# Optimization experiments

Hardware: AMD Instinct MI355X
Metric: run time of the kernel (lower is better)

Reference implementation:

```python
import jax, jax.numpy as jnp
import numpy as np

B, T, C, H = 2, 2048, 1024, 16
D = C // H
SCALE = 1.0 / np.sqrt(D).astype(np.float32)


def setup_inputs() -> dict:
    key = jax.random.key(0)
    kx, kq, kk, kv, ko = jax.random.split(key, 5)
    s = 1.0 / np.sqrt(C).astype(np.float32)
    return {
        "x": jax.random.normal(kx, (B, T, C), dtype=jnp.float32),
        "wq": jax.random.normal(kq, (C, C), dtype=jnp.float32) * s,
        "wk": jax.random.normal(kk, (C, C), dtype=jnp.float32) * s,
        "wv": jax.random.normal(kv, (C, C), dtype=jnp.float32) * s,
        "wo": jax.random.normal(ko, (C, C), dtype=jnp.float32) * s,
    }


def reference(x, wq, wk, wv, wo):
    # nn.Linear(y) = y @ W.T; weights stored [out, in]
    q = (x @ wq.T).reshape(B, T, H, D).transpose(0, 2, 1, 3)  # [B,H,T,D]
    k = (x @ wk.T).reshape(B, T, H, D).transpose(0, 2, 1, 3)
    v = (x @ wv.T).reshape(B, T, H, D).transpose(0, 2, 1, 3)
    scores = jnp.einsum("bhqd,bhkd->bhqk", q, k) * SCALE  # [B,H,T,T]
    causal = jnp.tril(jnp.ones((T, T), dtype=bool))
    scores = jnp.where(causal, scores, -jnp.inf)
    attn = jax.nn.softmax(scores, axis=-1)
    out = jnp.einsum("bhqk,bhkd->bhqd", attn, v)  # [B,H,T,D]
    out = out.transpose(0, 2, 1, 3).reshape(B, T, C)
    return out @ wo.T
```

## Files before the change

### kernel.cpp

```cpp
#include <hip/hip_runtime.h>
#include <hip/hip_bf16.h>

#define B_ 2
#define T_ 2048
#define C_ 1024
#define H_ 16
#define D_ 64
#define M_ (B_*T_)
#define SCALE_ 0.125f
#define LOG2E_ 1.44269504f
#define NEG_ (-1e30f)
#define THR_ 8.0f

typedef __bf16 bf16;
typedef __bf16 bf16x4 __attribute__((ext_vector_type(4)));
typedef __bf16 bf16x8 __attribute__((ext_vector_type(8)));
typedef float  f32x4  __attribute__((ext_vector_type(4)));

#define XB_ELEMS  ((size_t)M_*C_)
#define W_ELEMS   ((size_t)C_*C_)

__device__ __forceinline__ void glds16(const void* g, void* l) {
  __builtin_amdgcn_global_load_lds((const __attribute__((address_space(1))) void*)g,
                                   (__attribute__((address_space(3))) void*)l,
                                   16, 0, 0);
}

__global__ __launch_bounds__(256)
void cvt5(const float* __restrict__ x,  const float* __restrict__ wq,
          const float* __restrict__ wk, const float* __restrict__ wv,
          const float* __restrict__ wo, bf16* __restrict__ out,
          bf16* __restrict__ wodst) {
  int bid = blockIdx.x;
  const float* src; bf16* dst; size_t off;
  if (bid < 2048)      { src = x;  dst = out;                         off = (size_t)bid*2048; }
  else if (bid < 2560) { src = wq; dst = out + XB_ELEMS;              off = (size_t)(bid-2048)*2048; }
  else if (bid < 3072) { src = wk; dst = out + XB_ELEMS +   W_ELEMS;  off = (size_t)(bid-2560)*2048; }
  else if (bid < 3584) { src = wv; dst = out + XB_ELEMS + 2*W_ELEMS;  off = (size_t)(bid-3072)*2048; }
  else                 { src = wo; dst = wodst;                       off = (size_t)(bid-3584)*2048; }
  size_t i = off + (size_t)threadIdx.x * 8;
  f32x4 lo = *(const f32x4*)(src + i);
  f32x4 hi = *(const f32x4*)(src + i + 4);
  bf16x8 r;
  #pragma unroll
  for (int t = 0; t < 4; ++t) { r[t] = (bf16)lo[t]; r[t+4] = (bf16)hi[t]; }
  *(bf16x8*)(dst + i) = r;
}

template<int OUTMODE>
__global__ __launch_bounds__(256)
void gemm_nt(const bf16* __restrict__ Ab,
             const bf16* __restrict__ W0, const bf16* __restrict__ W1,
             const bf16* __restrict__ W2,
             void* __restrict__ O0v, void* __restrict__ O1v, void* __restrict__ O2v,
             int K) {
  __shared__ __align__(16) bf16 As[128*64];
  __shared__ __align__(16) bf16 Bs[128*64];

  const bf16* W = W0;
  void* Ov = O0v;
  bool vtrans = false;
  float oscale = 1.0f;
  if constexpr (OUTMODE == 0) {
    if (blockIdx.z == 0)      { oscale = SCALE_ * LOG2E_; }
    else if (blockIdx.z == 1) { W = W1; Ov = O1v; }
    else                      { W = W2; Ov = O2v; vtrans = true; }
  }

  const int m0 = blockIdx.y * 128, n0 = blockIdx.x * 128;
  const int tid = threadIdx.x, wid = tid >> 6, lane = tid & 63;
  const int wm = wid >> 1, wn = wid & 1;
  const int l15 = lane & 15, grp = lane >> 4;

  f32x4 acc[4][4] = {};

  const int lr8 = lane >> 3;
  const int lkswz = ((lane & 7) ^ lr8) * 8;
  const bf16* Ag = Ab + (size_t)(m0 + wid*8 + lr8) * K + lkswz;
  const bf16* Bg = W  + (size_t)(n0 + wid*8 + lr8) * K + lkswz;

  const int amRow = wm*64 + l15;
  const int bnRow = wn*64 + l15;
  const int swz = l15 & 7;

  for (int k0 = 0; k0 < K; k0 += 64) {
    __syncthreads();
    #pragma unroll
    for (int c = 0; c < 4; ++c) {
      glds16(Ag + (size_t)(c*32)*K + k0, As + (wid + c*4)*512);
      glds16(Bg + (size_t)(c*32)*K + k0, Bs + (wid + c*4)*512);
    }
    __syncthreads();

    #pragma unroll
    for (int ks = 0; ks < 2; ++ks) {
      const int aslot = ((ks*4 + grp) ^ swz) * 8;
      bf16x8 af[4], bfr[4];
      #pragma unroll
      for (int i = 0; i < 4; ++i) {
        af[i]  = *(const bf16x8*)(As + (amRow + i*16)*64 + aslot);
        bfr[i] = *(const bf16x8*)(Bs + (bnRow + i*16)*64 + aslot);
      }
      __builtin_amdgcn_s_setprio(1);
      #pragma unroll
      for (int i = 0; i < 4; ++i)
        #pragma unroll
        for (int j = 0; j < 4; ++j)
          acc[i][j] = __builtin_amdgcn_mfma_f32_16x16x32_bf16(af[i], bfr[j], acc[i][j], 0, 0, 0);
      __builtin_amdgcn_s_setprio(0);
    }
  }

  const int rBase = m0 + wm*64 + grp * 4;
  const int cBase = n0 + wn*64 + l15;
  #pragma unroll
  for (int fm = 0; fm < 4; ++fm) {
    #pragma unroll
    for (int fn = 0; fn < 4; ++fn) {
      #pragma unroll
      for (int j = 0; j < 4; ++j) {
        int m = rBase + fm*16 + j;
        int n = cBase + fn*16;
        if constexpr (OUTMODE == 0) {
          int b = m >> 11, t = m & 2047, h = n >> 6, d = n & 63;
          size_t idx = vtrans ? (((size_t)(b*H_ + h) * D_ + d) * T_ + t)
                              : (((size_t)(b*H_ + h) * T_ + t) * D_ + d);
          ((bf16*)Ov)[idx] = (bf16)(acc[fm][fn][j] * oscale);
        } else {
          ((float*)Ov)[(size_t)m * C_ + n] = acc[fm][fn][j];
        }
      }
    }
  }
}

#define LKV 72

__global__ __launch_bounds__(256)
void attn_fwd(const bf16* __restrict__ Q, const bf16* __restrict__ Km,
              const bf16* __restrict__ Vt, bf16* __restrict__ Oa) {
  __shared__ __align__(16) bf16 Ks [64*LKV];
  __shared__ __align__(16) bf16 Vts[64*LKV];
  __shared__ __align__(16) bf16 Ps [64*LKV];

  const int id = blockIdx.x;
  const int qt = 31 - (id >> 5);
  const int bh = id & 31;
  const int q0 = qt * 64;
  const int tid = threadIdx.x, wid = tid >> 6, lane = tid & 63;
  const int l15 = lane & 15;
  const int grp = lane >> 4;
  const int myrow4 = grp * 4;

  const bf16* Qb = Q  + (size_t)bh * T_ * D_;
  const bf16* Kb = Km + (size_t)bh * T_ * D_;
  const bf16* Vb = Vt + (size_t)bh * D_ * T_;

  const int ksr = tid >> 3, kskc = tid & 7;
  const int kSlot = grp * 8;
  const int b = bh >> 4, h = bh & 15;

  const int qrow = q0 + wid*16 + l15;
  bf16x8 aq0 = *(const bf16x8*)(Qb + (size_t)qrow*64 +      grp*8);
  bf16x8 aq1 = *(const bf16x8*)(Qb + (size_t)qrow*64 + 32 + grp*8);

  f32x4 oacc[4] = {};
  float m_s = NEG_, l_s = 0.f;

  bf16x8 kv_a = *(const bf16x8*)(Kb + (size_t)(ksr)*64      + kskc*8);
  bf16x8 kv_b = *(const bf16x8*)(Kb + (size_t)(ksr + 32)*64 + kskc*8);
  bf16x8 vt_a = *(const bf16x8*)(Vb + (size_t)(ksr     )*T_ + kskc*8);
  bf16x8 vt_b = *(const bf16x8*)(Vb + (size_t)(ksr + 32)*T_ + kskc*8);

  for (int kt = 0; kt <= qt; ++kt) {
    const int kv0 = kt * 64;

    __syncthreads();
    *(bf16x8*)(Ks  + ksr*LKV      + kskc*8) = kv_a;
    *(bf16x8*)(Ks  + (ksr+32)*LKV + kskc*8) = kv_b;
    *(bf16x8*)(Vts + ksr*LKV      + kskc*8) = vt_a;
    *(bf16x8*)(Vts + (ksr+32)*LKV + kskc*8) = vt_b;
    __syncthreads();

    {
      const int kn = (kt < qt) ? kv0 + 64 : kv0;
      kv_a = *(const bf16x8*)(Kb + (size_t)(kn + ksr)*64      + kskc*8);
      kv_b = *(const bf16x8*)(Kb + (size_t)(kn + ksr + 32)*64 + kskc*8);
      vt_a = *(const bf16x8*)(Vb + (size_t)(ksr     )*T_ + kn + kskc*8);
      vt_b = *(const bf16x8*)(Vb + (size_t)(ksr + 32)*T_ + kn + kskc*8);
    }

    f32x4 s[4];
    __builtin_amdgcn_s_setprio(1);
    #pragma unroll
    for (int n = 0; n < 4; ++n) {
      int row = n*16 + l15;
      bf16x8 bk0 = *(const bf16x8*)(Ks + row*LKV      + kSlot);
      bf16x8 bk1 = *(const bf16x8*)(Ks + row*LKV + 32 + kSlot);
      f32x4 a = {};
      a = __builtin_amdgcn_mfma_f32_16x16x32_bf16(bk0, aq0, a, 0, 0, 0);
      a = __builtin_amdgcn_mfma_f32_16x16x32_bf16(bk1, aq1, a, 0, 0, 0);
      s[n] = a;
    }
    __builtin_amdgcn_s_setprio(0);

    float pmax = NEG_;
    if (kt == qt) {
      #pragma unroll
      for (int n = 0; n < 4; ++n)
        #pragma unroll
        for (int j = 0; j < 4; ++j) {
          int kvg = kv0 + n*16 + myrow4 + j;
          float sv = (kvg <= qrow) ? s[n][j] : NEG_;
          s[n][j] = sv;
          pmax = fmaxf(pmax, sv);
        }
    } else {
      #pragma unroll
      for (int n = 0; n < 4; ++n)
        #pragma unroll
        for (int j = 0; j < 4; ++j) pmax = fmaxf(pmax, s[n][j]);
    }
    pmax = fmaxf(pmax, __shfl_xor(pmax, 16));
    pmax = fmaxf(pmax, __shfl_xor(pmax, 32));

    if (__any(pmax > m_s + THR_)) {
      float mnew = fmaxf(m_s, pmax);
      float scold = __builtin_amdgcn_exp2f(m_s - mnew);
      m_s = mnew;
      l_s *= scold;
      #pragma unroll
      for (int j = 0; j < 4; ++j) {
        float scj = __shfl(scold, myrow4 + j);
        #pragma unroll
        for (int n = 0; n < 4; ++n) oacc[n][j] *= scj;
      }
    }

    float ps = 0.f;
    #pragma unroll
    for (int n = 0; n < 4; ++n) {
      bf16x4 pw;
      #pragma unroll
      for (int j = 0; j < 4; ++j) {
        float p = __builtin_amdgcn_exp2f(s[n][j] - m_s);
        ps += p;
        pw[j] = (bf16)p;
      }
      *(bf16x4*)(Ps + (size_t)(wid*16 + l15)*LKV + n*16 + myrow4) = pw;
    }
    ps += __shfl_xor(ps, 16);
    ps += __shfl_xor(ps, 32);
    l_s += ps;

    asm volatile("s_waitcnt lgkmcnt(0)" ::: "memory");
    __builtin_amdgcn_sched_barrier(0);

    int parow = wid*16 + l15;
    bf16x8 pa0 = *(const bf16x8*)(Ps + parow*LKV      + kSlot);
    bf16x8 pa1 = *(const bf16x8*)(Ps + parow*LKV + 32 + kSlot);
    __builtin_amdgcn_s_setprio(1);
    #pragma unroll
    for (int n = 0; n < 4; ++n) {
      int vrow = n*16 + l15;
      bf16x8 bv0 = *(const bf16x8*)(Vts + vrow*LKV      + kSlot);
      bf16x8 bv1 = *(const bf16x8*)(Vts + vrow*LKV + 32 + kSlot);
      oacc[n] = __builtin_amdgcn_mfma_f32_16x16x32_bf16(pa0, bv0, oacc[n], 0, 0, 0);
      oacc[n] = __builtin_amdgcn_mfma_f32_16x16x32_bf16(pa1, bv1, oacc[n], 0, 0, 0);
    }
    __builtin_amdgcn_s_setprio(0);
  }

  const int tg = q0 + wid*16 + myrow4;
  #pragma unroll
  for (int j = 0; j < 4; ++j) {
    float lj = __shfl(l_s, myrow4 + j);
    float inv = 1.f / lj;
    int trow = tg + j;
    #pragma unroll
    for (int n = 0; n < 4; ++n) {
      int ch = h*64 + n*16 + l15;
      Oa[((size_t)(b*T_ + trow)) * C_ + ch] = (bf16)(oacc[n][j] * inv);
    }
  }
}

extern "C" void kernel_launch(void* const* d_in, const int* in_sizes, int n_in,
                              void* d_out, int out_size, void* d_ws, size_t ws_size,
                              hipStream_t stream) {
  const float* x  = (const float*)d_in[0];
  const float* wq = (const float*)d_in[1];
  const float* wk = (const float*)d_in[2];
  const float* wv = (const float*)d_in[3];
  const float* wo = (const float*)d_in[4];

  bf16* q  = (bf16*)d_ws;
  bf16* k  = q  + XB_ELEMS;
  bf16* v  = k  + XB_ELEMS;

  bf16* cvtbuf = (bf16*)d_out;
  bf16* xb  = cvtbuf;
  bf16* wqb = cvtbuf + XB_ELEMS;
  bf16* wkb = wqb + W_ELEMS;
  bf16* wvb = wkb + W_ELEMS;
  bf16* wob_stage = wvb + W_ELEMS;

  const bool bigws = ws_size >= (4*XB_ELEMS + W_ELEMS) * sizeof(bf16);
  bf16* ao  = bigws ? (v + XB_ELEMS) : xb;
  bf16* wob = bigws ? (v + XB_ELEMS + XB_ELEMS) : wob_stage;

  dim3 blk(256);
  cvt5<<<dim3(4096), blk, 0, stream>>>(x, wq, wk, wv, wo, cvtbuf, wob);
  gemm_nt<0><<<dim3(C_/128, M_/128, 3), blk, 0, stream>>>(xb, wqb, wkb, wvb,
                                                          q, k, v, C_);
  attn_fwd<<<dim3(1024), blk, 0, stream>>>(q, k, v, ao);
  bf16* aoSrc = ao;
  if (!bigws) {
    hipMemcpyAsync(q, xb,        XB_ELEMS * sizeof(bf16), hipMemcpyDeviceToDevice, stream);
    hipMemcpyAsync(k, wob_stage, W_ELEMS  * sizeof(bf16), hipMemcpyDeviceToDevice, stream);
    aoSrc = q; wob = k;
  }
  gemm_nt<1><<<dim3(C_/128, M_/128, 1), blk, 0, stream>>>(aoSrc, wob, nullptr, nullptr,
                                                          d_out, nullptr, nullptr, C_);
}
```

Before: 113.2 us.

## Split causal attention over KV range into two halves with combine kernel

Splits each query tile's causal KV loop into two roughly equal halves run by separate blocks (2048 blocks instead of 1024). Each half writes an unnormalized bf16 partial output plus per-row max and sum, and a new combine kernel merges them with log-sum-exp weights into the attention output. This targets load imbalance and low occupancy from the triangular causal work. In exchange it adds an extra kernel launch, an extra round trip of partial outputs through memory, and a larger workspace requirement; otherwise it falls back to the old path.

```diff
diff --git a/kernel.cpp b/kernel.cpp
--- a/kernel.cpp
+++ b/kernel.cpp
@@ -19,6 +19,8 @@
 
 #define XB_ELEMS  ((size_t)M_*C_)
 #define W_ELEMS   ((size_t)C_*C_)
+#define NSLOT     2048
+#define ML_FLOATS ((size_t)NSLOT*64*2)
 
 __device__ __forceinline__ void glds16(const void* g, void* l) {
   __builtin_amdgcn_global_load_lds((const __attribute__((address_space(1))) void*)g,
@@ -137,6 +139,202 @@
 #define LKV 72
 
 __global__ __launch_bounds__(256)
+void attn_split(const bf16* __restrict__ Q, const bf16* __restrict__ Km,
+                const bf16* __restrict__ Vt, bf16* __restrict__ pO,
+                float* __restrict__ ml) {
+  __shared__ __align__(16) bf16 Ks [64*LKV];
+  __shared__ __align__(16) bf16 Vts[64*LKV];
+  __shared__ __align__(16) bf16 Ps [64*LKV];
+
+  const int id = blockIdx.x;
+  const int qt = 31 - (id >> 6);
+  const int half = (id >> 5) & 1;
+  const int bh = id & 31;
+  const int q0 = qt * 64;
+  const int nl = (qt >> 1) + 1;
+  const int k0t = half ? nl : 0;
+  const int k1t = half ? (qt + 1) : nl;
+  const int slot = (qt*32 + bh)*2 + half;
+
+  const int tid = threadIdx.x, wid = tid >> 6, lane = tid & 63;
+  const int l15 = lane & 15;
+  const int grp = lane >> 4;
+  const int myrow4 = grp * 4;
+
+  if (k0t >= k1t) {
+    if (grp == 0 && wid < 4) {
+      int row = wid*16 + l15;
+      ml[(size_t)slot*128 + row*2    ] = NEG_;
+      ml[(size_t)slot*128 + row*2 + 1] = 0.f;
+    }
+    return;
+  }
+
+  const bf16* Qb = Q  + (size_t)bh * T_ * D_;
+  const bf16* Kb = Km + (size_t)bh * T_ * D_;
+  const bf16* Vb = Vt + (size_t)bh * D_ * T_;
+
+  const int ksr = tid >> 3, kskc = tid & 7;
+  const int kSlot = grp * 8;
+
+  const int qrow = q0 + wid*16 + l15;
+  bf16x8 aq0 = *(const bf16x8*)(Qb + (size_t)qrow*64 +      grp*8);
+  bf16x8 aq1 = *(const bf16x8*)(Qb + (size_t)qrow*64 + 32 + grp*8);
+
+  f32x4 oacc[4] = {};
+  float m_s = NEG_, l_s = 0.f;
+
+  const int kvS = k0t * 64;
+  bf16x8 kv_a = *(const bf16x8*)(Kb + (size_t)(kvS + ksr)*64      + kskc*8);
+  bf16x8 kv_b = *(const bf16x8*)(Kb + (size_t)(kvS + ksr + 32)*64 + kskc*8);
+  bf16x8 vt_a = *(const bf16x8*)(Vb + (size_t)(ksr     )*T_ + kvS + kskc*8);
+  bf16x8 vt_b = *(const bf16x8*)(Vb + (size_t)(ksr + 32)*T_ + kvS + kskc*8);
+
+  for (int kt = k0t; kt < k1t; ++kt) {
+    const int kv0 = kt * 64;
+
+    __syncthreads();
+    *(bf16x8*)(Ks  + ksr*LKV      + kskc*8) = kv_a;
+    *(bf16x8*)(Ks  + (ksr+32)*LKV + kskc*8) = kv_b;
+    *(bf16x8*)(Vts + ksr*LKV      + kskc*8) = vt_a;
+    *(bf16x8*)(Vts + (ksr+32)*LKV + kskc*8) = vt_b;
+    __syncthreads();
+
+    {
+      const int kn = (kt + 1 < k1t) ? kv0 + 64 : kv0;
+      kv_a = *(const bf16x8*)(Kb + (size_t)(kn + ksr)*64      + kskc*8);
+      kv_b = *(const bf16x8*)(Kb + (size_t)(kn + ksr + 32)*64 + kskc*8);
+      vt_a = *(const bf16x8*)(Vb + (size_t)(ksr     )*T_ + kn + kskc*8);
+      vt_b = *(const bf16x8*)(Vb + (size_t)(ksr + 32)*T_ + kn + kskc*8);
+    }
+
+    f32x4 s[4];
+    __builtin_amdgcn_s_setprio(1);
+    #pragma unroll
+    for (int n = 0; n < 4; ++n) {
+      int row = n*16 + l15;
+      bf16x8 bk0 = *(const bf16x8*)(Ks + row*LKV      + kSlot);
+      bf16x8 bk1 = *(const bf16x8*)(Ks + row*LKV + 32 + kSlot);
+      f32x4 a = {};
+      a = __builtin_amdgcn_mfma_f32_16x16x32_bf16(bk0, aq0, a, 0, 0, 0);
+      a = __builtin_amdgcn_mfma_f32_16x16x32_bf16(bk1, aq1, a, 0, 0, 0);
+      s[n] = a;
+    }
+    __builtin_amdgcn_s_setprio(0);
+
+    float pmax = NEG_;
+    if (kt == qt) {
+      #pragma unroll
+      for (int n = 0; n < 4; ++n)
+        #pragma unroll
+        for (int j = 0; j < 4; ++j) {
+          int kvg = kv0 + n*16 + myrow4 + j;
+          float sv = (kvg <= qrow) ? s[n][j] : NEG_;
+          s[n][j] = sv;
+          pmax = fmaxf(pmax, sv);
+        }
+    } else {
+      #pragma unroll
+      for (int n = 0; n < 4; ++n)
+        #pragma unroll
+        for (int j = 0; j < 4; ++j) pmax = fmaxf(pmax, s[n][j]);
+    }
+    pmax = fmaxf(pmax, __shfl_xor(pmax, 16));
+    pmax = fmaxf(pmax, __shfl_xor(pmax, 32));
+
+    if (__any(pmax > m_s + THR_)) {
+      float mnew = fmaxf(m_s, pmax);
+      float scold = __builtin_amdgcn_exp2f(m_s - mnew);
+      m_s = mnew;
+      l_s *= scold;
+      #pragma unroll
+      for (int j = 0; j < 4; ++j) {
+        float scj = __shfl(scold, myrow4 + j);
+        #pragma unroll
+        for (int n = 0; n < 4; ++n) oacc[n][j] *= scj;
+      }
+    }
+
+    float ps = 0.f;
+    #pragma unroll
+    for (int n = 0; n < 4; ++n) {
+      bf16x4 pw;
+      #pragma unroll
+      for (int j = 0; j < 4; ++j) {
+        float p = __builtin_amdgcn_exp2f(s[n][j] - m_s);
+        ps += p;
+        pw[j] = (bf16)p;
+      }
+      *(bf16x4*)(Ps + (size_t)(wid*16 + l15)*LKV + n*16 + myrow4) = pw;
+    }
+    ps += __shfl_xor(ps, 16);
+    ps += __shfl_xor(ps, 32);
+    l_s += ps;
+
+    asm volatile("s_waitcnt lgkmcnt(0)" ::: "memory");
+    __builtin_amdgcn_sched_barrier(0);
+
+    int parow = wid*16 + l15;
+    bf16x8 pa0 = *(const bf16x8*)(Ps + parow*LKV      + kSlot);
+    bf16x8 pa1 = *(const bf16x8*)(Ps + parow*LKV + 32 + kSlot);
+    __builtin_amdgcn_s_setprio(1);
+    #pragma unroll
+    for (int n = 0; n < 4; ++n) {
+      int vrow = n*16 + l15;
+      bf16x8 bv0 = *(const bf16x8*)(Vts + vrow*LKV      + kSlot);
+      bf16x8 bv1 = *(const bf16x8*)(Vts + vrow*LKV + 32 + kSlot);
+      oacc[n] = __builtin_amdgcn_mfma_f32_16x16x32_bf16(pa0, bv0, oacc[n], 0, 0, 0);
+      oacc[n] = __builtin_amdgcn_mfma_f32_16x16x32_bf16(pa1, bv1, oacc[n], 0, 0, 0);
+    }
+    __builtin_amdgcn_s_setprio(0);
+  }
+
+  bf16* po = pO + (size_t)slot * 4096;
+  #pragma unroll
+  for (int j = 0; j < 4; ++j) {
+    int row = wid*16 + myrow4 + j;
+    #pragma unroll
+    for (int n = 0; n < 4; ++n)
+      po[row*64 + n*16 + l15] = (bf16)oacc[n][j];
+  }
+  if (grp == 0) {
+    int row = wid*16 + l15;
+    ml[(size_t)slot*128 + row*2    ] = m_s;
+    ml[(size_t)slot*128 + row*2 + 1] = l_s;
+  }
+}
+
+__global__ __launch_bounds__(256)
+void combine(const bf16* __restrict__ pO, const float* __restrict__ ml,
+             bf16* __restrict__ ao) {
+  int g = blockIdx.x * 256 + threadIdx.x;
+  int pair = g >> 6, r = g & 63;
+  int qt = pair >> 5, bh = pair & 31;
+  int s1 = pair*2, s2 = pair*2 + 1;
+  float m1 = ml[(size_t)s1*128 + r*2], l1 = ml[(size_t)s1*128 + r*2 + 1];
+  float m2 = ml[(size_t)s2*128 + r*2], l2 = ml[(size_t)s2*128 + r*2 + 1];
+  float M  = fmaxf(m1, m2);
+  float w1 = __builtin_amdgcn_exp2f(m1 - M);
+  float w2 = __builtin_amdgcn_exp2f(m2 - M);
+  float inv = 1.f / (w1*l1 + w2*l2);
+  w1 *= inv; w2 *= inv;
+  const bf16* p1 = pO + (size_t)s1*4096 + r*64;
+  const bf16* p2 = pO + (size_t)s2*4096 + r*64;
+  int b = bh >> 4, h = bh & 15, t = qt*64 + r;
+  bf16* dst = ao + ((size_t)(b*T_ + t))*C_ + h*64;
+  #pragma unroll
+  for (int c = 0; c < 8; ++c) {
+    bf16x8 a = *(const bf16x8*)(p1 + c*8);
+    bf16x8 bq = *(const bf16x8*)(p2 + c*8);
+    bf16x8 o;
+    #pragma unroll
+    for (int j = 0; j < 8; ++j)
+      o[j] = (bf16)(w1*(float)a[j] + w2*(float)bq[j]);
+    *(bf16x8*)(dst + c*8) = o;
+  }
+}
+
+__global__ __launch_bounds__(256)
 void attn_fwd(const bf16* __restrict__ Q, const bf16* __restrict__ Km,
               const bf16* __restrict__ Vt, bf16* __restrict__ Oa) {
   __shared__ __align__(16) bf16 Ks [64*LKV];
@@ -174,7 +372,6 @@
 
   for (int kt = 0; kt <= qt; ++kt) {
     const int kv0 = kt * 64;
-
     __syncthreads();
     *(bf16x8*)(Ks  + ksr*LKV      + kskc*8) = kv_a;
     *(bf16x8*)(Ks  + (ksr+32)*LKV + kskc*8) = kv_b;
@@ -305,20 +502,31 @@
   bf16* wvb = wkb + W_ELEMS;
   bf16* wob_stage = wvb + W_ELEMS;
 
-  const bool bigws = ws_size >= (4*XB_ELEMS + W_ELEMS) * sizeof(bf16);
+  const size_t need_split = (4*XB_ELEMS + W_ELEMS)*sizeof(bf16) + ML_FLOATS*sizeof(float);
+  const size_t need_big   = (4*XB_ELEMS + W_ELEMS)*sizeof(bf16);
+  const bool splitws = ws_size >= need_split;
+  const bool bigws   = ws_size >= need_big;
+
   bf16* ao  = bigws ? (v + XB_ELEMS) : xb;
-  bf16* wob = bigws ? (v + XB_ELEMS + XB_ELEMS) : wob_stage;
+  bf16* wob = bigws ? (v + 2*XB_ELEMS) : wob_stage;
+  float* ml = (float*)(v + 2*XB_ELEMS + W_ELEMS);
 
   dim3 blk(256);
   cvt5<<<dim3(4096), blk, 0, stream>>>(x, wq, wk, wv, wo, cvtbuf, wob);
   gemm_nt<0><<<dim3(C_/128, M_/128, 3), blk, 0, stream>>>(xb, wqb, wkb, wvb,
                                                           q, k, v, C_);
-  attn_fwd<<<dim3(1024), blk, 0, stream>>>(q, k, v, ao);
   bf16* aoSrc = ao;
-  if (!bigws) {
-    hipMemcpyAsync(q, xb,        XB_ELEMS * sizeof(bf16), hipMemcpyDeviceToDevice, stream);
-    hipMemcpyAsync(k, wob_stage, W_ELEMS  * sizeof(bf16), hipMemcpyDeviceToDevice, stream);
-    aoSrc = q; wob = k;
+  if (splitws) {
+    bf16* pO = (bf16*)d_out;
+    attn_split<<<dim3(2048), blk, 0, stream>>>(q, k, v, pO, ml);
+    combine<<<dim3(256), blk, 0, stream>>>(pO, ml, ao);
+  } else {
+    attn_fwd<<<dim3(1024), blk, 0, stream>>>(q, k, v, ao);
+    if (!bigws) {
+      hipMemcpyAsync(q, xb,        XB_ELEMS * sizeof(bf16), hipMemcpyDeviceToDevice, stream);
+      hipMemcpyAsync(k, wob_stage, W_ELEMS  * sizeof(bf16), hipMemcpyDeviceToDevice, stream);
+      aoSrc = q; wob = k;
+    }
   }
   gemm_nt<1><<<dim3(C_/128, M_/128, 1), blk, 0, stream>>>(aoSrc, wob, nullptr, nullptr,
                                                           d_out, nullptr, nullptr, C_);
```

Result: slower. 125.0 us (+10.4%).

## Double-buffer attention K/V tiles via direct global-to-LDS loads with XOR swizzle

Applied to the files above, without the earlier changes.

The attention kernel stops staging K and V tiles through registers and instead issues direct global-to-LDS loads into two alternating LDS buffers, prefetching the next tile while the current one is computed. This removes one of the two block barriers per iteration along with the register copies. The padded LDS rows (stride 72) are replaced by unpadded 64-wide rows with an XOR swizzle on 16-byte chunks for K, V and P to avoid bank conflicts. Correctness relies on the async LDS loads being complete at the single barrier, and the double buffer raises LDS use per block.

```diff
diff --git a/kernel.cpp b/kernel.cpp
--- a/kernel.cpp
+++ b/kernel.cpp
@@ -134,14 +134,12 @@
   }
 }
 
-#define LKV 72
-
 __global__ __launch_bounds__(256)
 void attn_fwd(const bf16* __restrict__ Q, const bf16* __restrict__ Km,
               const bf16* __restrict__ Vt, bf16* __restrict__ Oa) {
-  __shared__ __align__(16) bf16 Ks [64*LKV];
-  __shared__ __align__(16) bf16 Vts[64*LKV];
-  __shared__ __align__(16) bf16 Ps [64*LKV];
+  __shared__ __align__(16) bf16 Kd[2][64*64];
+  __shared__ __align__(16) bf16 Vd[2][64*64];
+  __shared__ __align__(16) bf16 Ps[64*64];
 
   const int id = blockIdx.x;
   const int qt = 31 - (id >> 5);
@@ -151,14 +149,20 @@
   const int l15 = lane & 15;
   const int grp = lane >> 4;
   const int myrow4 = grp * 4;
+  const int sw = l15 & 7;
 
   const bf16* Qb = Q  + (size_t)bh * T_ * D_;
   const bf16* Kb = Km + (size_t)bh * T_ * D_;
   const bf16* Vb = Vt + (size_t)bh * D_ * T_;
 
-  const int ksr = tid >> 3, kskc = tid & 7;
-  const int kSlot = grp * 8;
   const int b = bh >> 4, h = bh & 15;
+
+  const int r8  = lane >> 3;
+  const int csw = ((lane & 7) ^ r8) * 8;
+  const bf16* KgA = Kb + (size_t)(wid*8     + r8)*64 + csw;
+  const bf16* KgB = Kb + (size_t)((wid+4)*8 + r8)*64 + csw;
+  const bf16* VgA = Vb + (size_t)(wid*8     + r8)*T_ + csw;
+  const bf16* VgB = Vb + (size_t)((wid+4)*8 + r8)*T_ + csw;
 
   const int qrow = q0 + wid*16 + l15;
   bf16x8 aq0 = *(const bf16x8*)(Qb + (size_t)qrow*64 +      grp*8);
@@ -167,36 +171,35 @@
   f32x4 oacc[4] = {};
   float m_s = NEG_, l_s = 0.f;
 
-  bf16x8 kv_a = *(const bf16x8*)(Kb + (size_t)(ksr)*64      + kskc*8);
-  bf16x8 kv_b = *(const bf16x8*)(Kb + (size_t)(ksr + 32)*64 + kskc*8);
-  bf16x8 vt_a = *(const bf16x8*)(Vb + (size_t)(ksr     )*T_ + kskc*8);
-  bf16x8 vt_b = *(const bf16x8*)(Vb + (size_t)(ksr + 32)*T_ + kskc*8);
+  glds16(KgA,  &Kd[0][wid*512]);
+  glds16(KgB,  &Kd[0][(wid+4)*512]);
+  glds16(VgA,  &Vd[0][wid*512]);
+  glds16(VgB,  &Vd[0][(wid+4)*512]);
 
   for (int kt = 0; kt <= qt; ++kt) {
     const int kv0 = kt * 64;
+    const int cur = kt & 1;
 
     __syncthreads();
-    *(bf16x8*)(Ks  + ksr*LKV      + kskc*8) = kv_a;
-    *(bf16x8*)(Ks  + (ksr+32)*LKV + kskc*8) = kv_b;
-    *(bf16x8*)(Vts + ksr*LKV      + kskc*8) = vt_a;
-    *(bf16x8*)(Vts + (ksr+32)*LKV + kskc*8) = vt_b;
-    __syncthreads();
-
-    {
-      const int kn = (kt < qt) ? kv0 + 64 : kv0;
-      kv_a = *(const bf16x8*)(Kb + (size_t)(kn + ksr)*64      + kskc*8);
-      kv_b = *(const bf16x8*)(Kb + (size_t)(kn + ksr + 32)*64 + kskc*8);
-      vt_a = *(const bf16x8*)(Vb + (size_t)(ksr     )*T_ + kn + kskc*8);
-      vt_b = *(const bf16x8*)(Vb + (size_t)(ksr + 32)*T_ + kn + kskc*8);
-    }
+
+    if (kt < qt) {
+      const int kn = kv0 + 64;
+      glds16(KgA + (size_t)kn*64, &Kd[cur^1][wid*512]);
+      glds16(KgB + (size_t)kn*64, &Kd[cur^1][(wid+4)*512]);
+      glds16(VgA + kn,            &Vd[cur^1][wid*512]);
+      glds16(VgB + kn,            &Vd[cur^1][(wid+4)*512]);
+    }
+
+    const bf16* Kc = Kd[cur];
+    const bf16* Vc = Vd[cur];
 
     f32x4 s[4];
     __builtin_amdgcn_s_setprio(1);
     #pragma unroll
     for (int n = 0; n < 4; ++n) {
       int row = n*16 + l15;
-      bf16x8 bk0 = *(const bf16x8*)(Ks + row*LKV      + kSlot);
-      bf16x8 bk1 = *(const bf16x8*)(Ks + row*LKV + 32 + kSlot);
+      bf16x8 bk0 = *(const bf16x8*)(Kc + row*64 + ((grp     ^ sw)*8));
+      bf16x8 bk1 = *(const bf16x8*)(Kc + row*64 + (((grp|4) ^ sw)*8));
       f32x4 a = {};
       a = __builtin_amdgcn_mfma_f32_16x16x32_bf16(bk0, aq0, a, 0, 0, 0);
       a = __builtin_amdgcn_mfma_f32_16x16x32_bf16(bk1, aq1, a, 0, 0, 0);
@@ -237,6 +240,7 @@
       }
     }
 
+    const int prow = wid*16 + l15;
     float ps = 0.f;
     #pragma unroll
     for (int n = 0; n < 4; ++n) {
@@ -247,7 +251,8 @@
         ps += p;
         pw[j] = (bf16)p;
       }
-      *(bf16x4*)(Ps + (size_t)(wid*16 + l15)*LKV + n*16 + myrow4) = pw;
+      int sl = (2*n + (grp >> 1)) ^ sw;
+      *(bf16x4*)(Ps + prow*64 + sl*8 + (grp & 1)*4) = pw;
     }
     ps += __shfl_xor(ps, 16);
     ps += __shfl_xor(ps, 32);
@@ -256,15 +261,14 @@
     asm volatile("s_waitcnt lgkmcnt(0)" ::: "memory");
     __builtin_amdgcn_sched_barrier(0);
 
-    int parow = wid*16 + l15;
-    bf16x8 pa0 = *(const bf16x8*)(Ps + parow*LKV      + kSlot);
-    bf16x8 pa1 = *(const bf16x8*)(Ps + parow*LKV + 32 + kSlot);
+    bf16x8 pa0 = *(const bf16x8*)(Ps + prow*64 + ((grp     ^ sw)*8));
+    bf16x8 pa1 = *(const bf16x8*)(Ps + prow*64 + (((grp|4) ^ sw)*8));
     __builtin_amdgcn_s_setprio(1);
     #pragma unroll
     for (int n = 0; n < 4; ++n) {
       int vrow = n*16 + l15;
-      bf16x8 bv0 = *(const bf16x8*)(Vts + vrow*LKV      + kSlot);
-      bf16x8 bv1 = *(const bf16x8*)(Vts + vrow*LKV + 32 + kSlot);
+      bf16x8 bv0 = *(const bf16x8*)(Vc + vrow*64 + ((grp     ^ sw)*8));
+      bf16x8 bv1 = *(const bf16x8*)(Vc + vrow*64 + (((grp|4) ^ sw)*8));
       oacc[n] = __builtin_amdgcn_mfma_f32_16x16x32_bf16(pa0, bv0, oacc[n], 0, 0, 0);
       oacc[n] = __builtin_amdgcn_mfma_f32_16x16x32_bf16(pa1, bv1, oacc[n], 0, 0, 0);
     }
@@ -307,7 +311,7 @@
 
   const bool bigws = ws_size >= (4*XB_ELEMS + W_ELEMS) * sizeof(bf16);
   bf16* ao  = bigws ? (v + XB_ELEMS) : xb;
-  bf16* wob = bigws ? (v + XB_ELEMS + XB_ELEMS) : wob_stage;
+  bf16* wob = bigws ? (v + 2*XB_ELEMS) : wob_stage;
 
   dim3 blk(256);
   cvt5<<<dim3(4096), blk, 0, stream>>>(x, wq, wk, wv, wo, cvtbuf, wob);
```

After: 114.5 us. Within noise of the previous version (+1.1%).
